# Performance work log

Hardware: AMD Instinct MI355X
Metric: run time of the kernel (lower is better)

The kernel has to match this reference:

```python
import jax, jax.numpy as jnp
import numpy as np

B, H, W, C = 8, 64, 64, 768
NUM_HEADS = 12
KSIZE = 3
DILATIONS = (1, 2, 3)
ND = len(DILATIONS)
HEAD_DIM = C // NUM_HEADS  # 64
SCALE = HEAD_DIM ** (-0.5)


def setup_inputs() -> dict:
    key = jax.random.key(0)
    kx, kqkv, kpw, kpb = jax.random.split(key, 4)
    x = jax.random.normal(kx, (B, H, W, C), dtype=jnp.float32)
    # 1x1 conv qkv: weight [3C, C] (no bias, qkv_bias=False)
    qkv_w = jax.random.normal(kqkv, (3 * C, C), dtype=jnp.float32) * (C ** -0.5)
    # nn.Linear proj: weight [C, C], bias [C]
    proj_w = jax.random.normal(kpw, (C, C), dtype=jnp.float32) * (C ** -0.5)
    proj_b = jax.random.normal(kpb, (C,), dtype=jnp.float32) * 0.01
    return {"x": x, "qkv_w": qkv_w, "proj_w": proj_w, "proj_b": proj_b}


def _unfold(t, k, dil):
    # t: [B, d, H, W] -> [B, d, k*k, H, W]; matches nn.Unfold(k, dil, pad=dil*(k-1)//2)
    b, d, h, w = t.shape
    pad = dil * (k - 1) // 2
    tp = jnp.pad(t, ((0, 0), (0, 0), (pad, pad), (pad, pad)))
    patches = [tp[:, :, i * dil:i * dil + h, j * dil:j * dil + w]
               for i in range(k) for j in range(k)]
    return jnp.stack(patches, axis=2)


def reference(x, qkv_w, proj_w, proj_b):
    b, h, w, c = x.shape
    d = c // ND                 # channels per dilation group
    hpd = NUM_HEADS // ND       # heads per dilation group
    xc = x.transpose(0, 3, 1, 2)                      # [B, C, H, W]
    qkv = jnp.einsum('bchw,oc->bohw', xc, qkv_w)      # [B, 3C, H, W]
    qkv = qkv.reshape(b, 3, ND, d, h, w)
    outs = []
    for i, dil in enumerate(DILATIONS):
        q = qkv[:, 0, i].reshape(b, hpd, HEAD_DIM, h, w)
        ku = _unfold(qkv[:, 1, i], KSIZE, dil).reshape(b, hpd, HEAD_DIM, KSIZE * KSIZE, h, w)
        vu = _unfold(qkv[:, 2, i], KSIZE, dil).reshape(b, hpd, HEAD_DIM, KSIZE * KSIZE, h, w)
        attn = jnp.einsum('bnchw,bncKhw->bnKhw', q, ku) * SCALE
        attn = jax.nn.softmax(attn, axis=2)           # over the k*k neighborhood
        o = jnp.einsum('bnKhw,bncKhw->bnchw', attn, vu)  # [B, hpd, hd, H, W]
        outs.append(o.transpose(0, 3, 4, 1, 2).reshape(b, h, w, d))
    y = jnp.concatenate(outs, axis=-1)                # dilation-major channel order
    y = y + x                                          # DWConvAttention branch is identity
    y = jnp.einsum('bhwc,oc->bhwo', y, proj_w) + proj_b
    return y
```

## Files before the change

### kernel.cpp

```cpp
#include <hip/hip_runtime.h>
#include <hip/hip_bf16.h>

#define CC 768
#define MM 32768
#define NQKV 2304
#define SCALE_ 0.125f

typedef __bf16 bf16x8 __attribute__((ext_vector_type(8)));
typedef float f32x4 __attribute__((ext_vector_type(4)));
typedef unsigned short ushort8_t __attribute__((ext_vector_type(8)));

static __device__ __forceinline__ float bf2f(unsigned short u) {
  return __uint_as_float(((unsigned int)u) << 16);
}
static __device__ __forceinline__ unsigned short f2bf(float f) {
  __hip_bfloat16 t = __float2bfloat16(f);
  return __builtin_bit_cast(unsigned short, t);
}

__global__ void cvt_kernel(const float* __restrict__ in,
                           __hip_bfloat16* __restrict__ out, int n4) {
  int i = blockIdx.x * blockDim.x + threadIdx.x;
  if (i >= n4) return;
  float4 v = reinterpret_cast<const float4*>(in)[i];
  ushort4 o;
  o.x = f2bf(v.x); o.y = f2bf(v.y); o.z = f2bf(v.z); o.w = f2bf(v.w);
  reinterpret_cast<ushort4*>(out)[i] = o;
}

template <int MODE>
__global__ __launch_bounds__(256) void gemm_bf16_kernel(
    const __hip_bfloat16* __restrict__ A,
    const __hip_bfloat16* __restrict__ Bw,
    void* __restrict__ outp,
    const float* __restrict__ bias,
    int M, int N, int K) {
  __shared__ __hip_bfloat16 lA[3][128 * 32];
  __shared__ __hip_bfloat16 lB[3][128 * 32];

  const int nBN = N >> 7;
  const int cpx = gridDim.x >> 3;
  const int bid = ((int)blockIdx.x & 7) * cpx + ((int)blockIdx.x >> 3);
  const int bm = bid / nBN;
  const int bn = bid % nBN;
  const int tid = threadIdx.x;
  const int lane = tid & 63;
  const int wv = tid >> 6;
  const int wr = wv >> 1;
  const int wc = wv & 1;

  f32x4 acc[4][4] = {};

  const int srow = wv * 16 + (lane >> 2);
  const int scol = ((lane & 3) ^ ((lane >> 3) & 3)) * 8;
  const size_t Abase = (size_t)(bm * 128) * K;
  const size_t Bbase = (size_t)(bn * 128) * K;

  const int frow = lane & 15;
  const int g = lane >> 4;
  const int fcol = (g ^ ((frow >> 1) & 3)) * 8;

  auto stage = [&](int buf, int t) {
    const int k0 = t << 5;
#pragma unroll
    for (int c = 0; c < 2; ++c) {
      const __hip_bfloat16* gA = A + Abase + (size_t)(c * 64 + srow) * K + k0 + scol;
      __hip_bfloat16* sA = &lA[buf][(c * 64 + wv * 16) * 32];
      __builtin_amdgcn_global_load_lds(
          (const __attribute__((address_space(1))) void*)gA,
          (__attribute__((address_space(3))) void*)sA, 16, 0, 0);
      const __hip_bfloat16* gB = Bw + Bbase + (size_t)(c * 64 + srow) * K + k0 + scol;
      __hip_bfloat16* sB = &lB[buf][(c * 64 + wv * 16) * 32];
      __builtin_amdgcn_global_load_lds(
          (const __attribute__((address_space(1))) void*)gB,
          (__attribute__((address_space(3))) void*)sB, 16, 0, 0);
    }
  };

  const int nt = K >> 5;
  stage(0, 0);
  if (nt > 1) stage(1, 1);

  int rd = 0;
  int st = 2;
  for (int t = 0; t < nt; ++t) {
    if (t + 1 < nt) asm volatile("s_waitcnt vmcnt(4)" ::: "memory");
    else            asm volatile("s_waitcnt vmcnt(0)" ::: "memory");
    __builtin_amdgcn_s_barrier();
    asm volatile("" ::: "memory");

    bf16x8 af[4], bfr[4];
#pragma unroll
    for (int m = 0; m < 4; ++m)
      af[m] = *reinterpret_cast<const bf16x8*>(&lA[rd][(wr * 64 + m * 16 + frow) * 32 + fcol]);
#pragma unroll
    for (int n = 0; n < 4; ++n)
      bfr[n] = *reinterpret_cast<const bf16x8*>(&lB[rd][(wc * 64 + n * 16 + frow) * 32 + fcol]);

    if (t + 2 < nt) stage(st, t + 2);

#pragma unroll
    for (int m = 0; m < 4; ++m)
#pragma unroll
      for (int n = 0; n < 4; ++n)
        acc[m][n] = __builtin_amdgcn_mfma_f32_16x16x32_bf16(af[m], bfr[n], acc[m][n], 0, 0, 0);

    rd = (rd == 2) ? 0 : rd + 1;
    st = (st == 2) ? 0 : st + 1;
  }

  const int r0 = (lane >> 4) * 4;
  const int cc_ = lane & 15;
#pragma unroll
  for (int m = 0; m < 4; ++m) {
#pragma unroll
    for (int n = 0; n < 4; ++n) {
      const int grow = bm * 128 + wr * 64 + m * 16 + r0;
      const int gcol = bn * 128 + wc * 64 + n * 16 + cc_;
      if (MODE == 1) {
        __hip_bfloat16* outT = (__hip_bfloat16*)outp;
        ushort4 pk;
        pk.x = f2bf(acc[m][n][0]);
        pk.y = f2bf(acc[m][n][1]);
        pk.z = f2bf(acc[m][n][2]);
        pk.w = f2bf(acc[m][n][3]);
        *reinterpret_cast<ushort4*>(outT + (size_t)gcol * M + grow) = pk;
      } else {
        float* outF = (float*)outp;
        const float bv = bias ? bias[gcol] : 0.f;
#pragma unroll
        for (int r = 0; r < 4; ++r)
          outF[(size_t)(grow + r) * N + gcol] = acc[m][n][r] + bv;
      }
    }
  }
}

__global__ __launch_bounds__(256) void attn_kernel(
    const unsigned short* __restrict__ qkvT,
    const unsigned short* __restrict__ xres,
    unsigned short* __restrict__ y) {
  const int hh = blockIdx.x >> 7;
  const int head = hh >> 1;
  const int half = hh & 1;
  const int p = ((blockIdx.x & 127) << 8) + threadIdx.x;
  const int h = (p >> 6) & 63;
  const int w = p & 63;
  const int grp = head >> 2;
  const int dil = grp + 1;
  const int chq = grp * 256 + (head & 3) * 64;

  int voff[9];
  bool valid[9];
#pragma unroll
  for (int t = 0; t < 9; ++t) {
    const int di = t / 3 - 1, dj = t % 3 - 1;
    valid[t] = ((unsigned)(h + di * dil) < 64u) && ((unsigned)(w + dj * dil) < 64u);
    voff[t] = p + (di * 64 + dj) * dil + 256;
  }
  const int voffq = p + 256;

  const unsigned short* qb = qkvT + (size_t)chq * MM - 256;
  const unsigned short* kb = qkvT + (size_t)(768 + chq) * MM - 256;

  float l[9] = {};
#pragma unroll 1
  for (int cb = 0; cb < 16; ++cb) {
    unsigned short qv[4];
    unsigned short kv[4][9];
#pragma unroll
    for (int i = 0; i < 4; ++i) qv[i] = qb[voffq + i * MM];
#pragma unroll
    for (int i = 0; i < 4; ++i)
#pragma unroll
      for (int t = 0; t < 9; ++t) kv[i][t] = kb[voff[t] + i * MM];
#pragma unroll
    for (int i = 0; i < 4; ++i) {
      const float qf = bf2f(qv[i]);
#pragma unroll
      for (int t = 0; t < 9; ++t)
        l[t] = fmaf(qf, bf2f(kv[i][t]), l[t]);
    }
    qb += 4 * MM;
    kb += 4 * MM;
  }

#pragma unroll
  for (int t = 0; t < 9; ++t) l[t] = valid[t] ? l[t] * SCALE_ : 0.f;
  float mx = l[0];
#pragma unroll
  for (int t = 1; t < 9; ++t) mx = fmaxf(mx, l[t]);
  float den = 0.f;
#pragma unroll
  for (int t = 0; t < 9; ++t) {
    const float e = __expf(l[t] - mx);
    den += e;
    l[t] = valid[t] ? e : 0.f;
  }
  const float inv = 1.f / den;
#pragma unroll
  for (int t = 0; t < 9; ++t) l[t] *= inv;

  const int cho = chq + half * 32;
  const unsigned short* vb = qkvT + (size_t)(1536 + cho) * MM - 256;
  float vout[32];
#pragma unroll 1
  for (int cb = 0; cb < 8; ++cb) {
    unsigned short vv[4][9];
#pragma unroll
    for (int i = 0; i < 4; ++i)
#pragma unroll
      for (int t = 0; t < 9; ++t) vv[i][t] = vb[voff[t] + i * MM];
#pragma unroll
    for (int i = 0; i < 4; ++i) {
      float acc = 0.f;
#pragma unroll
      for (int t = 0; t < 9; ++t)
        acc = fmaf(l[t], bf2f(vv[i][t]), acc);
      vout[cb * 4 + i] = acc;
    }
    vb += 4 * MM;
  }

  const ushort8_t* xr = reinterpret_cast<const ushort8_t*>(xres + (size_t)p * CC + cho);
  ushort8_t* yr = reinterpret_cast<ushort8_t*>(y + (size_t)p * CC + cho);
#pragma unroll
  for (int k = 0; k < 4; ++k) {
    const ushort8_t xa = xr[k];
    ushort8_t o;
#pragma unroll
    for (int j = 0; j < 8; ++j)
      o[j] = f2bf(vout[8 * k + j] + bf2f(xa[j]));
    yr[k] = o;
  }
}

extern "C" void kernel_launch(void* const* d_in, const int* in_sizes, int n_in,
                              void* d_out, int out_size, void* d_ws, size_t ws_size,
                              hipStream_t stream) {
  const float* x = (const float*)d_in[0];
  const float* qkv_w = (const float*)d_in[1];
  const float* proj_w = (const float*)d_in[2];
  const float* proj_b = (const float*)d_in[3];
  float* out = (float*)d_out;

  char* ws = (char*)d_ws;
  __hip_bfloat16* xb = (__hip_bfloat16*)(ws);
  __hip_bfloat16* qkvT = (__hip_bfloat16*)(ws + 50331648);
  __hip_bfloat16* wqkvb = (__hip_bfloat16*)(ws + 201326592);
  __hip_bfloat16* wprojb = (__hip_bfloat16*)(ws + 204865536);
  __hip_bfloat16* ybuf = xb;

  cvt_kernel<<<(MM * CC / 4 + 255) / 256, 256, 0, stream>>>(x, xb, MM * CC / 4);
  cvt_kernel<<<(NQKV * CC / 4 + 255) / 256, 256, 0, stream>>>(qkv_w, wqkvb, NQKV * CC / 4);
  cvt_kernel<<<(CC * CC / 4 + 255) / 256, 256, 0, stream>>>(proj_w, wprojb, CC * CC / 4);

  gemm_bf16_kernel<1><<<(MM / 128) * (NQKV / 128), 256, 0, stream>>>(
      xb, wqkvb, (void*)qkvT, nullptr, MM, NQKV, CC);

  attn_kernel<<<24 * 128, 256, 0, stream>>>(
      (const unsigned short*)qkvT, (const unsigned short*)xb,
      (unsigned short*)ybuf);

  gemm_bf16_kernel<2><<<(MM / 128) * (CC / 128), 256, 0, stream>>>(
      ybuf, wprojb, (void*)out, proj_b, MM, CC, CC);
}
```

Baseline: 385.7 us.

## Replace GEMM with 256x256-tile, 8-wave, finely interleaved load/MFMA pipeline

Replaces the 128x128-tile, 4-wave, triple-buffered GEMM with a 256x256-tile, 512-thread kernel that uses 64-wide K slices and double buffering. Global-to-LDS loads are split into half-tile stages and interleaved between eight MFMA sub-blocks, with barriers and s_setprio raising wave priority during MFMA phases. The larger tile raises arithmetic intensity and cuts redundant global reads. In exchange it uses much more LDS and registers per block, launches fewer blocks (e.g. 384 for the projection GEMM), and adds many barriers.

```diff
diff --git a/kernel.cpp b/kernel.cpp
--- a/kernel.cpp
+++ b/kernel.cpp
@@ -17,6 +17,12 @@
   __hip_bfloat16 t = __float2bfloat16(f);
   return __builtin_bit_cast(unsigned short, t);
 }
+
+#define FENCE() asm volatile("" ::: "memory")
+#define BAR() do { FENCE(); __builtin_amdgcn_s_barrier(); FENCE(); } while (0)
+#define GLDS(src, dst) __builtin_amdgcn_global_load_lds( \
+    (const __attribute__((address_space(1))) void*)(src), \
+    (__attribute__((address_space(3))) void*)(dst), 16, 0, 0)
 
 __global__ void cvt_kernel(const float* __restrict__ in,
                            __hip_bfloat16* __restrict__ out, int n4) {
@@ -29,16 +35,16 @@
 }
 
 template <int MODE>
-__global__ __launch_bounds__(256) void gemm_bf16_kernel(
+__global__ __launch_bounds__(512, 2) void gemm256_kernel(
     const __hip_bfloat16* __restrict__ A,
     const __hip_bfloat16* __restrict__ Bw,
     void* __restrict__ outp,
     const float* __restrict__ bias,
     int M, int N, int K) {
-  __shared__ __hip_bfloat16 lA[3][128 * 32];
-  __shared__ __hip_bfloat16 lB[3][128 * 32];
-
-  const int nBN = N >> 7;
+  __shared__ __hip_bfloat16 lA[2][256 * 64];
+  __shared__ __hip_bfloat16 lB[2][256 * 64];
+
+  const int nBN = N >> 8;
   const int cpx = gridDim.x >> 3;
   const int bid = ((int)blockIdx.x & 7) * cpx + ((int)blockIdx.x >> 3);
   const int bm = bid / nBN;
@@ -46,77 +52,199 @@
   const int tid = threadIdx.x;
   const int lane = tid & 63;
   const int wv = tid >> 6;
-  const int wr = wv >> 1;
-  const int wc = wv & 1;
-
-  f32x4 acc[4][4] = {};
-
-  const int srow = wv * 16 + (lane >> 2);
-  const int scol = ((lane & 3) ^ ((lane >> 3) & 3)) * 8;
-  const size_t Abase = (size_t)(bm * 128) * K;
-  const size_t Bbase = (size_t)(bn * 128) * K;
-
-  const int frow = lane & 15;
+  const int wr = wv >> 2;
+  const int wn = wv & 3;
+
+  const size_t Abase = (size_t)(bm * 256) * K;
+  const size_t Bbase = (size_t)(bn * 256) * K;
+
+  const int srow8 = lane >> 3;
+  const int sslot = (lane & 7) ^ srow8;
+
+  const int fr = lane & 15;
   const int g = lane >> 4;
-  const int fcol = (g ^ ((frow >> 1) & 3)) * 8;
-
-  auto stage = [&](int buf, int t) {
-    const int k0 = t << 5;
-#pragma unroll
-    for (int c = 0; c < 2; ++c) {
-      const __hip_bfloat16* gA = A + Abase + (size_t)(c * 64 + srow) * K + k0 + scol;
-      __hip_bfloat16* sA = &lA[buf][(c * 64 + wv * 16) * 32];
-      __builtin_amdgcn_global_load_lds(
-          (const __attribute__((address_space(1))) void*)gA,
-          (__attribute__((address_space(3))) void*)sA, 16, 0, 0);
-      const __hip_bfloat16* gB = Bw + Bbase + (size_t)(c * 64 + srow) * K + k0 + scol;
-      __hip_bfloat16* sB = &lB[buf][(c * 64 + wv * 16) * 32];
-      __builtin_amdgcn_global_load_lds(
-          (const __attribute__((address_space(1))) void*)gB,
-          (__attribute__((address_space(3))) void*)sB, 16, 0, 0);
+  const int sw = lane & 7;
+
+  f32x4 acc[8][4] = {};
+
+  auto stageA = [&](int slot, int half, int kt) {
+#pragma unroll
+    for (int i = 0; i < 2; ++i) {
+      const int rb = half * 128 + wv * 16 + i * 8;
+      const __hip_bfloat16* src =
+          A + Abase + (size_t)(rb + srow8) * K + (kt << 6) + (sslot << 3);
+      GLDS(src, &lA[slot][rb << 6]);
     }
   };
-
-  const int nt = K >> 5;
-  stage(0, 0);
-  if (nt > 1) stage(1, 1);
-
-  int rd = 0;
-  int st = 2;
-  for (int t = 0; t < nt; ++t) {
-    if (t + 1 < nt) asm volatile("s_waitcnt vmcnt(4)" ::: "memory");
-    else            asm volatile("s_waitcnt vmcnt(0)" ::: "memory");
-    __builtin_amdgcn_s_barrier();
-    asm volatile("" ::: "memory");
-
-    bf16x8 af[4], bfr[4];
-#pragma unroll
-    for (int m = 0; m < 4; ++m)
-      af[m] = *reinterpret_cast<const bf16x8*>(&lA[rd][(wr * 64 + m * 16 + frow) * 32 + fcol]);
-#pragma unroll
-    for (int n = 0; n < 4; ++n)
-      bfr[n] = *reinterpret_cast<const bf16x8*>(&lB[rd][(wc * 64 + n * 16 + frow) * 32 + fcol]);
-
-    if (t + 2 < nt) stage(st, t + 2);
-
-#pragma unroll
-    for (int m = 0; m < 4; ++m)
-#pragma unroll
-      for (int n = 0; n < 4; ++n)
-        acc[m][n] = __builtin_amdgcn_mfma_f32_16x16x32_bf16(af[m], bfr[n], acc[m][n], 0, 0, 0);
-
-    rd = (rd == 2) ? 0 : rd + 1;
-    st = (st == 2) ? 0 : st + 1;
+  auto stageB = [&](int slot, int half, int kt) {
+#pragma unroll
+    for (int i = 0; i < 2; ++i) {
+      const int rb = half * 128 + wv * 16 + i * 8;
+      const __hip_bfloat16* src =
+          Bw + Bbase + (size_t)(rb + srow8) * K + (kt << 6) + (sslot << 3);
+      GLDS(src, &lB[slot][rb << 6]);
+    }
+  };
+  auto ldA = [&](int slot, int m, int ks) -> bf16x8 {
+    const int row = wr * 128 + m * 16 + fr;
+    const int s = (ks * 4 + g) ^ sw;
+    return *reinterpret_cast<const bf16x8*>(&lA[slot][(row << 6) + (s << 3)]);
+  };
+  auto ldB = [&](int slot, int n, int ks) -> bf16x8 {
+    const int row = wn * 64 + n * 16 + fr;
+    const int s = (ks * 4 + g) ^ sw;
+    return *reinterpret_cast<const bf16x8*>(&lB[slot][(row << 6) + (s << 3)]);
+  };
+
+  const int nit = K >> 7;
+
+  stageA(0, 0, 0); stageA(0, 1, 0); stageB(0, 0, 0); stageB(0, 1, 0);
+  stageA(1, 0, 1);
+  asm volatile("s_waitcnt vmcnt(2)" ::: "memory");
+  BAR();
+
+  bf16x8 a4[4][2], bA[2][2], bB[2][2];
+
+  for (int t = 0; t < nit; ++t) {
+    const int k1 = 2 * t + 1, k2 = 2 * t + 2, k3 = 2 * t + 3;
+    const bool more = (t + 1 < nit);
+
+#pragma unroll
+    for (int m = 0; m < 4; ++m) { a4[m][0] = ldA(0, m, 0); a4[m][1] = ldA(0, m, 1); }
+#pragma unroll
+    for (int n = 0; n < 2; ++n) { bA[n][0] = ldB(0, n, 0); bA[n][1] = ldB(0, n, 1); }
+    stageA(1, 1, k1);
+    BAR();
+    __builtin_amdgcn_s_setprio(1);
+#pragma unroll
+    for (int m = 0; m < 4; ++m)
+#pragma unroll
+      for (int n = 0; n < 2; ++n)
+#pragma unroll
+        for (int ks = 0; ks < 2; ++ks)
+          acc[m][n] = __builtin_amdgcn_mfma_f32_16x16x32_bf16(a4[m][ks], bA[n][ks], acc[m][n], 0, 0, 0);
+    __builtin_amdgcn_s_setprio(0);
+    BAR();
+
+#pragma unroll
+    for (int n = 0; n < 2; ++n) { bB[n][0] = ldB(0, n + 2, 0); bB[n][1] = ldB(0, n + 2, 1); }
+    stageB(1, 0, k1);
+    BAR();
+    __builtin_amdgcn_s_setprio(1);
+#pragma unroll
+    for (int m = 0; m < 4; ++m)
+#pragma unroll
+      for (int n = 0; n < 2; ++n)
+#pragma unroll
+        for (int ks = 0; ks < 2; ++ks)
+          acc[m][n + 2] = __builtin_amdgcn_mfma_f32_16x16x32_bf16(a4[m][ks], bB[n][ks], acc[m][n + 2], 0, 0, 0);
+    __builtin_amdgcn_s_setprio(0);
+    BAR();
+
+#pragma unroll
+    for (int m = 0; m < 4; ++m) { a4[m][0] = ldA(0, m + 4, 0); a4[m][1] = ldA(0, m + 4, 1); }
+    stageB(1, 1, k1);
+    BAR();
+    __builtin_amdgcn_s_setprio(1);
+#pragma unroll
+    for (int m = 0; m < 4; ++m)
+#pragma unroll
+      for (int n = 0; n < 2; ++n)
+#pragma unroll
+        for (int ks = 0; ks < 2; ++ks)
+          acc[m + 4][n + 2] = __builtin_amdgcn_mfma_f32_16x16x32_bf16(a4[m][ks], bB[n][ks], acc[m + 4][n + 2], 0, 0, 0);
+    __builtin_amdgcn_s_setprio(0);
+    BAR();
+
+#pragma unroll
+    for (int n = 0; n < 2; ++n) { bA[n][0] = ldB(0, n, 0); bA[n][1] = ldB(0, n, 1); }
+    if (more) stageA(0, 0, k2);
+    BAR();
+    __builtin_amdgcn_s_setprio(1);
+#pragma unroll
+    for (int m = 0; m < 4; ++m)
+#pragma unroll
+      for (int n = 0; n < 2; ++n)
+#pragma unroll
+        for (int ks = 0; ks < 2; ++ks)
+          acc[m + 4][n] = __builtin_amdgcn_mfma_f32_16x16x32_bf16(a4[m][ks], bA[n][ks], acc[m + 4][n], 0, 0, 0);
+    __builtin_amdgcn_s_setprio(0);
+    if (more) { asm volatile("s_waitcnt vmcnt(2)" ::: "memory"); }
+    else      { asm volatile("s_waitcnt vmcnt(0)" ::: "memory"); }
+    BAR();
+
+#pragma unroll
+    for (int m = 0; m < 4; ++m) { a4[m][0] = ldA(1, m, 0); a4[m][1] = ldA(1, m, 1); }
+#pragma unroll
+    for (int n = 0; n < 2; ++n) { bA[n][0] = ldB(1, n, 0); bA[n][1] = ldB(1, n, 1); }
+    if (more) stageA(0, 1, k2);
+    BAR();
+    __builtin_amdgcn_s_setprio(1);
+#pragma unroll
+    for (int m = 0; m < 4; ++m)
+#pragma unroll
+      for (int n = 0; n < 2; ++n)
+#pragma unroll
+        for (int ks = 0; ks < 2; ++ks)
+          acc[m][n] = __builtin_amdgcn_mfma_f32_16x16x32_bf16(a4[m][ks], bA[n][ks], acc[m][n], 0, 0, 0);
+    __builtin_amdgcn_s_setprio(0);
+    BAR();
+
+#pragma unroll
+    for (int n = 0; n < 2; ++n) { bB[n][0] = ldB(1, n + 2, 0); bB[n][1] = ldB(1, n + 2, 1); }
+    if (more) stageB(0, 0, k2);
+    BAR();
+    __builtin_amdgcn_s_setprio(1);
+#pragma unroll
+    for (int m = 0; m < 4; ++m)
+#pragma unroll
+      for (int n = 0; n < 2; ++n)
+#pragma unroll
+        for (int ks = 0; ks < 2; ++ks)
+          acc[m][n + 2] = __builtin_amdgcn_mfma_f32_16x16x32_bf16(a4[m][ks], bB[n][ks], acc[m][n + 2], 0, 0, 0);
+    __builtin_amdgcn_s_setprio(0);
+    BAR();
+
+#pragma unroll
+    for (int m = 0; m < 4; ++m) { a4[m][0] = ldA(1, m + 4, 0); a4[m][1] = ldA(1, m + 4, 1); }
+    if (more) stageB(0, 1, k2);
+    BAR();
+    __builtin_amdgcn_s_setprio(1);
+#pragma unroll
+    for (int m = 0; m < 4; ++m)
+#pragma unroll
+      for (int n = 0; n < 2; ++n)
+#pragma unroll
+        for (int ks = 0; ks < 2; ++ks)
+          acc[m + 4][n + 2] = __builtin_amdgcn_mfma_f32_16x16x32_bf16(a4[m][ks], bB[n][ks], acc[m + 4][n + 2], 0, 0, 0);
+    __builtin_amdgcn_s_setprio(0);
+    BAR();
+
+#pragma unroll
+    for (int n = 0; n < 2; ++n) { bA[n][0] = ldB(1, n, 0); bA[n][1] = ldB(1, n, 1); }
+    if (more) stageA(1, 0, k3);
+    BAR();
+    __builtin_amdgcn_s_setprio(1);
+#pragma unroll
+    for (int m = 0; m < 4; ++m)
+#pragma unroll
+      for (int n = 0; n < 2; ++n)
+#pragma unroll
+        for (int ks = 0; ks < 2; ++ks)
+          acc[m + 4][n] = __builtin_amdgcn_mfma_f32_16x16x32_bf16(a4[m][ks], bA[n][ks], acc[m + 4][n], 0, 0, 0);
+    __builtin_amdgcn_s_setprio(0);
+    if (more) { asm volatile("s_waitcnt vmcnt(2)" ::: "memory"); }
+    BAR();
   }
 
   const int r0 = (lane >> 4) * 4;
   const int cc_ = lane & 15;
 #pragma unroll
-  for (int m = 0; m < 4; ++m) {
+  for (int m = 0; m < 8; ++m) {
 #pragma unroll
     for (int n = 0; n < 4; ++n) {
-      const int grow = bm * 128 + wr * 64 + m * 16 + r0;
-      const int gcol = bn * 128 + wc * 64 + n * 16 + cc_;
+      const int grow = bm * 256 + wr * 128 + m * 16 + r0;
+      const int gcol = bn * 256 + wn * 64 + n * 16 + cc_;
       if (MODE == 1) {
         __hip_bfloat16* outT = (__hip_bfloat16*)outp;
         ushort4 pk;
@@ -255,13 +383,13 @@
   cvt_kernel<<<(NQKV * CC / 4 + 255) / 256, 256, 0, stream>>>(qkv_w, wqkvb, NQKV * CC / 4);
   cvt_kernel<<<(CC * CC / 4 + 255) / 256, 256, 0, stream>>>(proj_w, wprojb, CC * CC / 4);
 
-  gemm_bf16_kernel<1><<<(MM / 128) * (NQKV / 128), 256, 0, stream>>>(
+  gemm256_kernel<1><<<(MM / 256) * (NQKV / 256), 512, 0, stream>>>(
       xb, wqkvb, (void*)qkvT, nullptr, MM, NQKV, CC);
 
   attn_kernel<<<24 * 128, 256, 0, stream>>>(
       (const unsigned short*)qkvT, (const unsigned short*)xb,
       (unsigned short*)ybuf);
 
-  gemm_bf16_kernel<2><<<(MM / 128) * (CC / 128), 256, 0, stream>>>(
+  gemm256_kernel<2><<<(MM / 256) * (CC / 256), 512, 0, stream>>>(
       ybuf, wprojb, (void*)out, proj_b, MM, CC, CC);
 }
```

After: 401.7 us. +4.2%, slower.

## Add 256x256-tile 8-wave GEMM with ping-pong staging for the QKV projection

Applied to the files above, without the earlier changes.

Adds a new GEMM kernel for the QKV projection with 256x256 output tiles, 512 threads, K-step 64 and an XOR-swizzled LDS layout. Loading of half-tiles is interleaved with MFMA blocks behind barriers and s_setprio. Larger tiles increase operand reuse and cut global and LDS traffic per flop, and the interleaving tries to hide load latency. The cost is much higher register use (128 accumulator floats per lane), more barriers per iteration, and fewer blocks in the grid. The proj GEMM keeps the old 128-tile kernel under a new name.

```diff
diff --git a/kernel.cpp b/kernel.cpp
--- a/kernel.cpp
+++ b/kernel.cpp
@@ -17,6 +17,12 @@
   __hip_bfloat16 t = __float2bfloat16(f);
   return __builtin_bit_cast(unsigned short, t);
 }
+
+#define FENCE() asm volatile("" ::: "memory")
+#define BAR() do { FENCE(); __builtin_amdgcn_s_barrier(); FENCE(); } while (0)
+#define GLDS(src, dst) __builtin_amdgcn_global_load_lds( \
+    (const __attribute__((address_space(1))) void*)(src), \
+    (__attribute__((address_space(3))) void*)(dst), 16, 0, 0)
 
 __global__ void cvt_kernel(const float* __restrict__ in,
                            __hip_bfloat16* __restrict__ out, int n4) {
@@ -29,7 +35,188 @@
 }
 
 template <int MODE>
-__global__ __launch_bounds__(256) void gemm_bf16_kernel(
+__global__ __launch_bounds__(512, 2) void gemm256_kernel(
+    const __hip_bfloat16* __restrict__ A,
+    const __hip_bfloat16* __restrict__ Bw,
+    void* __restrict__ outp,
+    const float* __restrict__ bias,
+    int M, int N, int K) {
+  __shared__ __hip_bfloat16 lA[2][2][128 * 64];
+  __shared__ __hip_bfloat16 lB[2][2][128 * 64];
+
+  const int nBN = N >> 8;
+  const int cpx = gridDim.x >> 3;
+  const int bid = ((int)blockIdx.x & 7) * cpx + ((int)blockIdx.x >> 3);
+  const int bm = bid / nBN;
+  const int bn = bid % nBN;
+  const int tid = threadIdx.x;
+  const int lane = tid & 63;
+  const int wv = tid >> 6;
+  const int wr = wv >> 2;
+  const int wn = wv & 3;
+
+  const size_t Abase = (size_t)(bm * 256) * K;
+  const size_t Bbase = (size_t)(bn * 256) * K;
+
+  const int srow8 = lane >> 3;
+  const int sslot = (lane & 7) ^ srow8;
+
+  const int fr = lane & 15;
+  const int g = lane >> 4;
+  const int sw = lane & 7;
+
+  f32x4 acc[8][4] = {};
+
+  auto stageA = [&](int slot, int half, int kt) {
+#pragma unroll
+    for (int i = 0; i < 2; ++i) {
+      const int lr = wv * 16 + i * 8 + srow8;
+      const int gr = ((lr >> 6) << 7) + half * 64 + (lr & 63);
+      const __hip_bfloat16* src =
+          A + Abase + (size_t)gr * K + (kt << 6) + (sslot << 3);
+      GLDS(src, &lA[slot][half][(wv * 16 + i * 8) << 6]);
+    }
+  };
+  auto stageB = [&](int slot, int half, int kt) {
+#pragma unroll
+    for (int i = 0; i < 2; ++i) {
+      const int lr = wv * 16 + i * 8 + srow8;
+      const int gr = ((lr >> 5) << 6) + half * 32 + (lr & 31);
+      const __hip_bfloat16* src =
+          Bw + Bbase + (size_t)gr * K + (kt << 6) + (sslot << 3);
+      GLDS(src, &lB[slot][half][(wv * 16 + i * 8) << 6]);
+    }
+  };
+  auto ldA = [&](int slot, int m, int ks) -> bf16x8 {
+    const int lr = wr * 64 + (m & 3) * 16 + fr;
+    const int s = (ks * 4 + g) ^ sw;
+    return *reinterpret_cast<const bf16x8*>(&lA[slot][m >> 2][(lr << 6) + (s << 3)]);
+  };
+  auto ldB = [&](int slot, int n, int ks) -> bf16x8 {
+    const int lr = wn * 32 + (n & 1) * 16 + fr;
+    const int s = (ks * 4 + g) ^ sw;
+    return *reinterpret_cast<const bf16x8*>(&lB[slot][n >> 1][(lr << 6) + (s << 3)]);
+  };
+
+  const int nit = K >> 7;
+
+  stageA(0, 0, 0); stageA(0, 1, 0); stageB(0, 0, 0); stageB(0, 1, 0);
+  stageA(1, 0, 1); stageB(1, 1, 1); stageA(1, 1, 1);
+  asm volatile("s_waitcnt vmcnt(6)" ::: "memory");
+  BAR();
+
+  bf16x8 a4[4][2], bA[2][2], bB[2][2];
+
+#define MFMA_BLK(AM, BN, ACCM, ACCN)                                          \
+  __builtin_amdgcn_s_setprio(1);                                              \
+  _Pragma("unroll")                                                           \
+  for (int m = 0; m < 4; ++m)                                                 \
+    _Pragma("unroll")                                                         \
+    for (int n = 0; n < 2; ++n)                                               \
+      _Pragma("unroll")                                                       \
+      for (int ks = 0; ks < 2; ++ks)                                          \
+        acc[(ACCM) + m][(ACCN) + n] = __builtin_amdgcn_mfma_f32_16x16x32_bf16(\
+            AM[m][ks], BN[n][ks], acc[(ACCM) + m][(ACCN) + n], 0, 0, 0);      \
+  __builtin_amdgcn_s_setprio(0);
+
+  for (int t = 0; t < nit; ++t) {
+    const int k1 = 2 * t + 1, k2 = 2 * t + 2, k3 = 2 * t + 3;
+    const bool more = (t + 1 < nit);
+
+#pragma unroll
+    for (int m = 0; m < 4; ++m) { a4[m][0] = ldA(0, m, 0); a4[m][1] = ldA(0, m, 1); }
+#pragma unroll
+    for (int n = 0; n < 2; ++n) { bA[n][0] = ldB(0, n, 0); bA[n][1] = ldB(0, n, 1); }
+    stageB(1, 0, k1);
+    BAR();
+    MFMA_BLK(a4, bA, 0, 0)
+    BAR();
+
+#pragma unroll
+    for (int n = 0; n < 2; ++n) { bB[n][0] = ldB(0, n + 2, 0); bB[n][1] = ldB(0, n + 2, 1); }
+    if (more) stageA(0, 0, k2);
+    BAR();
+    MFMA_BLK(a4, bB, 0, 2)
+    BAR();
+
+#pragma unroll
+    for (int m = 0; m < 4; ++m) { a4[m][0] = ldA(0, m + 4, 0); a4[m][1] = ldA(0, m + 4, 1); }
+    if (more) stageB(0, 1, k2);
+    BAR();
+    MFMA_BLK(a4, bB, 4, 2)
+    BAR();
+
+#pragma unroll
+    for (int n = 0; n < 2; ++n) { bA[n][0] = ldB(0, n, 0); bA[n][1] = ldB(0, n, 1); }
+    if (more) stageA(0, 1, k2);
+    BAR();
+    MFMA_BLK(a4, bA, 4, 0)
+    if (more) { asm volatile("s_waitcnt vmcnt(6)" ::: "memory"); }
+    else      { asm volatile("s_waitcnt vmcnt(0)" ::: "memory"); }
+    BAR();
+
+#pragma unroll
+    for (int m = 0; m < 4; ++m) { a4[m][0] = ldA(1, m, 0); a4[m][1] = ldA(1, m, 1); }
+#pragma unroll
+    for (int n = 0; n < 2; ++n) { bA[n][0] = ldB(1, n, 0); bA[n][1] = ldB(1, n, 1); }
+    if (more) stageB(0, 0, k2);
+    BAR();
+    MFMA_BLK(a4, bA, 0, 0)
+    BAR();
+
+#pragma unroll
+    for (int n = 0; n < 2; ++n) { bB[n][0] = ldB(1, n + 2, 0); bB[n][1] = ldB(1, n + 2, 1); }
+    if (more) stageA(1, 0, k3);
+    BAR();
+    MFMA_BLK(a4, bB, 0, 2)
+    BAR();
+
+#pragma unroll
+    for (int m = 0; m < 4; ++m) { a4[m][0] = ldA(1, m + 4, 0); a4[m][1] = ldA(1, m + 4, 1); }
+    if (more) stageB(1, 1, k3);
+    BAR();
+    MFMA_BLK(a4, bB, 4, 2)
+    BAR();
+
+#pragma unroll
+    for (int n = 0; n < 2; ++n) { bA[n][0] = ldB(1, n, 0); bA[n][1] = ldB(1, n, 1); }
+    if (more) stageA(1, 1, k3);
+    BAR();
+    MFMA_BLK(a4, bA, 4, 0)
+    if (more) { asm volatile("s_waitcnt vmcnt(6)" ::: "memory"); }
+    BAR();
+  }
+#undef MFMA_BLK
+
+  const int r0 = (lane >> 4) * 4;
+  const int cc_ = lane & 15;
+#pragma unroll
+  for (int m = 0; m < 8; ++m) {
+#pragma unroll
+    for (int n = 0; n < 4; ++n) {
+      const int grow = bm * 256 + wr * 128 + m * 16 + r0;
+      const int gcol = bn * 256 + wn * 64 + n * 16 + cc_;
+      if (MODE == 1) {
+        __hip_bfloat16* outT = (__hip_bfloat16*)outp;
+        ushort4 pk;
+        pk.x = f2bf(acc[m][n][0]);
+        pk.y = f2bf(acc[m][n][1]);
+        pk.z = f2bf(acc[m][n][2]);
+        pk.w = f2bf(acc[m][n][3]);
+        *reinterpret_cast<ushort4*>(outT + (size_t)gcol * M + grow) = pk;
+      } else {
+        float* outF = (float*)outp;
+        const float bv = bias ? bias[gcol] : 0.f;
+#pragma unroll
+        for (int r = 0; r < 4; ++r)
+          outF[(size_t)(grow + r) * N + gcol] = acc[m][n][r] + bv;
+      }
+    }
+  }
+}
+
+template <int MODE>
+__global__ __launch_bounds__(256) void gemm128_kernel(
     const __hip_bfloat16* __restrict__ A,
     const __hip_bfloat16* __restrict__ Bw,
     void* __restrict__ outp,
@@ -65,15 +252,9 @@
 #pragma unroll
     for (int c = 0; c < 2; ++c) {
       const __hip_bfloat16* gA = A + Abase + (size_t)(c * 64 + srow) * K + k0 + scol;
-      __hip_bfloat16* sA = &lA[buf][(c * 64 + wv * 16) * 32];
-      __builtin_amdgcn_global_load_lds(
-          (const __attribute__((address_space(1))) void*)gA,
-          (__attribute__((address_space(3))) void*)sA, 16, 0, 0);
+      GLDS(gA, &lA[buf][(c * 64 + wv * 16) * 32]);
       const __hip_bfloat16* gB = Bw + Bbase + (size_t)(c * 64 + srow) * K + k0 + scol;
-      __hip_bfloat16* sB = &lB[buf][(c * 64 + wv * 16) * 32];
-      __builtin_amdgcn_global_load_lds(
-          (const __attribute__((address_space(1))) void*)gB,
-          (__attribute__((address_space(3))) void*)sB, 16, 0, 0);
+      GLDS(gB, &lB[buf][(c * 64 + wv * 16) * 32]);
     }
   };
 
@@ -87,7 +268,7 @@
     if (t + 1 < nt) asm volatile("s_waitcnt vmcnt(4)" ::: "memory");
     else            asm volatile("s_waitcnt vmcnt(0)" ::: "memory");
     __builtin_amdgcn_s_barrier();
-    asm volatile("" ::: "memory");
+    FENCE();
 
     bf16x8 af[4], bfr[4];
 #pragma unroll
@@ -255,13 +436,13 @@
   cvt_kernel<<<(NQKV * CC / 4 + 255) / 256, 256, 0, stream>>>(qkv_w, wqkvb, NQKV * CC / 4);
   cvt_kernel<<<(CC * CC / 4 + 255) / 256, 256, 0, stream>>>(proj_w, wprojb, CC * CC / 4);
 
-  gemm_bf16_kernel<1><<<(MM / 128) * (NQKV / 128), 256, 0, stream>>>(
+  gemm256_kernel<1><<<(MM / 256) * (NQKV / 256), 512, 0, stream>>>(
       xb, wqkvb, (void*)qkvT, nullptr, MM, NQKV, CC);
 
   attn_kernel<<<24 * 128, 256, 0, stream>>>(
       (const unsigned short*)qkvT, (const unsigned short*)xb,
       (unsigned short*)ybuf);
 
-  gemm_bf16_kernel<2><<<(MM / 128) * (CC / 128), 256, 0, stream>>>(
+  gemm128_kernel<2><<<(MM / 128) * (CC / 128), 256, 0, stream>>>(
       ybuf, wprojb, (void*)out, proj_b, MM, CC, CC);
 }
```

New measurement: 404.8 us. 1.05x slower.
